# Optimization experiments

Hardware: AMD Instinct MI355X
Metric: run time of the kernel (lower is better)

## Reference

```python
import jax, jax.numpy as jnp
import numpy as np

IN_DIM = 135909   # input feature vocab (Amazon-670K style)
OUT_DIM = 670091  # output classes
D = 128           # hardcoded embedding dim in the module
B = 256           # batch size
T = 100           # active features per sample (summed bag-of-features)


def setup_inputs() -> dict:
    key = jax.random.key(0)
    ks = jax.random.split(key, 6)
    x = jax.random.randint(ks[0], (B, T), 0, IN_DIM)
    y = jax.random.randint(ks[1], (B,), 0, OUT_DIM)
    # nn.Embedding(IN+1, 128, padding_idx=IN): last row is the zero padding row
    emb_table = jax.random.normal(ks[2], (IN_DIM + 1, D), jnp.float32) * 0.01
    emb_table = emb_table.at[IN_DIM].set(0.0)
    stdv = 1.0 / np.sqrt(IN_DIM)
    bias = jax.random.uniform(ks[3], (D,), jnp.float32, -stdv, stdv)
    # LSHSoftmax dense parameters: per-class weight [OUT, D] and bias [OUT]
    W = jax.random.normal(ks[4], (OUT_DIM, D), jnp.float32) * (1.0 / np.sqrt(D))
    b_out = jnp.zeros((OUT_DIM,), jnp.float32)
    return {"x": x, "y": y, "freeze": 0, "slide": 0,
            "emb_table": emb_table, "bias": bias, "W": W, "b_out": b_out}


def reference(x, y, freeze, slide, emb_table, bias, W, b_out):
    # raw_emb = sum over the feature indices (bag-of-features embedding sum)
    raw = jnp.sum(emb_table[x], axis=1)                      # [B, D]
    emb = raw / jnp.linalg.norm(raw, axis=1, keepdims=True)  # L2 normalize
    query = jax.nn.relu(emb + bias)                          # [B, D]
    # LSHSoftmax exact (slide=0 / full) path: dense softmax cross-entropy
    logits = query @ W.T + b_out                             # [B, OUT]
    logp = jax.nn.log_softmax(logits, axis=-1)
    loss = -jnp.mean(jnp.take_along_axis(logp, y[:, None], axis=1))
    return loss
```

## Files before the change

kernel.cpp:

```cpp
#include <hip/hip_runtime.h>
#include <hip/hip_bf16.h>

#define IN_DIMX 135909
#define OUT_DIMX 670091
#define DDIM 128
#define BATCH 256
#define TFEAT 100
#define NBLK 512
#define NCHUNK ((OUT_DIMX + 63) / 64)

typedef __bf16 bf16_t;
typedef __attribute__((ext_vector_type(8))) __bf16 bf16x8;
typedef __attribute__((ext_vector_type(4))) __bf16 bf16x4;
typedef __attribute__((ext_vector_type(4))) float f32x4;

__global__ void k_query(const int* __restrict__ x, const float* __restrict__ emb,
                        const float* __restrict__ bias, float* __restrict__ qf,
                        bf16_t* __restrict__ qb) {
    const int row = blockIdx.x;
    const int t = threadIdx.x;
    __shared__ int sidx[TFEAT];
    if (t < TFEAT) sidx[t] = x[row * TFEAT + t];
    __syncthreads();
    float s = 0.f;
    #pragma unroll 10
    for (int i = 0; i < TFEAT; ++i) {
        s += emb[(size_t)sidx[i] * DDIM + t];
    }
    float sq = s * s;
    #pragma unroll
    for (int off = 1; off < 64; off <<= 1) sq += __shfl_xor(sq, off, 64);
    __shared__ float wred[2];
    if ((threadIdx.x & 63) == 0) wred[threadIdx.x >> 6] = sq;
    __syncthreads();
    const float tot = wred[0] + wred[1];
    float q = s / sqrtf(tot) + bias[t];
    q = fmaxf(q, 0.f);
    qf[row * DDIM + t] = q;
    qb[row * DDIM + t] = (bf16_t)q;
}

__global__ __launch_bounds__(256, 2)
void k_lse(const float* __restrict__ W, const float* __restrict__ b_out,
           const bf16_t* __restrict__ qb, float* __restrict__ partials) {
    __shared__ bf16_t lds[2][64 * DDIM];
    const int tid = threadIdx.x;
    const int lane = tid & 63;
    const int w = tid >> 6;
    const int l15 = lane & 15;
    const int l4 = lane >> 4;

    bf16x8 a[4][4];
    #pragma unroll
    for (int mt = 0; mt < 4; ++mt)
        #pragma unroll
        for (int ks = 0; ks < 4; ++ks)
            a[mt][ks] = *(const bf16x8*)(qb + (w * 64 + mt * 16 + l15) * DDIM + ks * 32 + 8 * l4);

    float rs[4][4];
    #pragma unroll
    for (int mt = 0; mt < 4; ++mt)
        #pragma unroll
        for (int r = 0; r < 4; ++r) rs[mt][r] = 0.f;

    const int srow = tid >> 5;
    const int scol = (tid & 31) * 4;
    const int c16  = (tid & 31) >> 1;
    const int half = (tid & 1) * 4;

    f32x4 wr[8];
    float bo_n[4];

    auto issue = [&](int ch) {
        const int cb = ch * 64;
        #pragma unroll
        for (int j = 0; j < 8; ++j) {
            int r = cb + j * 8 + srow;
            r = (r < OUT_DIMX) ? r : 0;
            wr[j] = *(const f32x4*)(W + (size_t)r * DDIM + scol);
        }
        #pragma unroll
        for (int nt = 0; nt < 4; ++nt) {
            int c = cb + nt * 16 + l15;
            c = (c < OUT_DIMX) ? c : 0;
            bo_n[nt] = b_out[c];
        }
    };

    auto convwrite = [&](int cur) {
        #pragma unroll
        for (int j = 0; j < 8; ++j) {
            const int row = j * 8 + srow;
            const int sp = row * 16 + (c16 ^ (row & 7));
            bf16x4 v;
            v[0] = (bf16_t)wr[j][0]; v[1] = (bf16_t)wr[j][1];
            v[2] = (bf16_t)wr[j][2]; v[3] = (bf16_t)wr[j][3];
            *(bf16x4*)(&lds[cur][sp * 8 + half]) = v;
        }
    };

    int cur = 0;
    issue(blockIdx.x);
    for (int ch = blockIdx.x; ch < NCHUNK; ch += NBLK) {
        float bo_c[4];
        #pragma unroll
        for (int nt = 0; nt < 4; ++nt) bo_c[nt] = bo_n[nt];

        convwrite(cur);
        __syncthreads();
        __builtin_amdgcn_sched_barrier(0);
        if (ch + NBLK < NCHUNK) issue(ch + NBLK);

        f32x4 acc[4][4];
        #pragma unroll
        for (int mt = 0; mt < 4; ++mt)
            #pragma unroll
            for (int nt = 0; nt < 4; ++nt) acc[mt][nt] = (f32x4){0.f, 0.f, 0.f, 0.f};

        #pragma unroll
        for (int ks = 0; ks < 4; ++ks) {
            bf16x8 b[4];
            #pragma unroll
            for (int nt = 0; nt < 4; ++nt) {
                const int row = nt * 16 + l15;
                const int sp = row * 16 + ((ks * 4 + l4) ^ (row & 7));
                b[nt] = *(const bf16x8*)(&lds[cur][sp * 8]);
            }
            #pragma unroll
            for (int nt = 0; nt < 4; ++nt)
                #pragma unroll
                for (int mt = 0; mt < 4; ++mt)
                    acc[mt][nt] = __builtin_amdgcn_mfma_f32_16x16x32_bf16(
                        a[mt][ks], b[nt], acc[mt][nt], 0, 0, 0);
        }

        const int cbase = ch * 64;
        if (cbase + 64 <= OUT_DIMX) {
            #pragma unroll
            for (int nt = 0; nt < 4; ++nt)
                #pragma unroll
                for (int mt = 0; mt < 4; ++mt)
                    #pragma unroll
                    for (int r = 0; r < 4; ++r)
                        rs[mt][r] += __expf(acc[mt][nt][r] + bo_c[nt]);
        } else {
            #pragma unroll
            for (int nt = 0; nt < 4; ++nt) {
                const bool valid = (cbase + nt * 16 + l15 < OUT_DIMX);
                #pragma unroll
                for (int mt = 0; mt < 4; ++mt)
                    #pragma unroll
                    for (int r = 0; r < 4; ++r)
                        rs[mt][r] += valid ? __expf(acc[mt][nt][r] + bo_c[nt]) : 0.f;
            }
        }
        cur ^= 1;
    }

    #pragma unroll
    for (int mt = 0; mt < 4; ++mt)
        #pragma unroll
        for (int r = 0; r < 4; ++r) {
            float v = rs[mt][r];
            v += __shfl_xor(v, 1, 64);
            v += __shfl_xor(v, 2, 64);
            v += __shfl_xor(v, 4, 64);
            v += __shfl_xor(v, 8, 64);
            if (l15 == 0) {
                const int rowb = w * 64 + mt * 16 + l4 * 4 + r;
                partials[(size_t)rowb * NBLK + blockIdx.x] = v;
            }
        }
}

__global__ void k_ydot(const int* __restrict__ y, const float* __restrict__ qf,
                       const float* __restrict__ W, const float* __restrict__ b_out,
                       float* __restrict__ logity) {
    const int i = blockIdx.x;
    const int lane = threadIdx.x;
    const int yi = y[i];
    const float* wrow = W + (size_t)yi * DDIM;
    const float* qrow = qf + i * DDIM;
    float s = qrow[lane] * wrow[lane] + qrow[lane + 64] * wrow[lane + 64];
    #pragma unroll
    for (int off = 1; off < 64; off <<= 1) s += __shfl_xor(s, off, 64);
    if (lane == 0) logity[i] = s + b_out[yi];
}

__global__ void k_rowlse(const float* __restrict__ partials,
                         const float* __restrict__ logity,
                         float* __restrict__ rowloss) {
    const int i = blockIdx.x;
    const int lane = threadIdx.x;
    float s = 0.f;
    #pragma unroll
    for (int k = 0; k < NBLK / 64; ++k)
        s += partials[(size_t)i * NBLK + k * 64 + lane];
    #pragma unroll
    for (int off = 1; off < 64; off <<= 1) s += __shfl_xor(s, off, 64);
    if (lane == 0) rowloss[i] = logf(s) - logity[i];
}

__global__ void k_final(const float* __restrict__ rowloss, float* __restrict__ out) {
    const int i = threadIdx.x;
    float t = rowloss[i];
    #pragma unroll
    for (int off = 1; off < 64; off <<= 1) t += __shfl_xor(t, off, 64);
    __shared__ float wred[4];
    if ((threadIdx.x & 63) == 0) wred[threadIdx.x >> 6] = t;
    __syncthreads();
    if (threadIdx.x == 0)
        out[0] = (wred[0] + wred[1] + wred[2] + wred[3]) * (1.0f / (float)BATCH);
}

extern "C" void kernel_launch(void* const* d_in, const int* in_sizes, int n_in,
                              void* d_out, int out_size, void* d_ws, size_t ws_size,
                              hipStream_t stream) {
    const int*   x     = (const int*)d_in[0];
    const int*   y     = (const int*)d_in[1];
    const float* emb   = (const float*)d_in[4];
    const float* bias  = (const float*)d_in[5];
    const float* W     = (const float*)d_in[6];
    const float* b_out = (const float*)d_in[7];
    float* out = (float*)d_out;

    char* ws = (char*)d_ws;
    bf16_t* qb       = (bf16_t*)(ws);
    float*  qf       = (float*)(ws + 65536);
    float*  logity   = (float*)(ws + 196608);
    float*  rowloss  = (float*)(ws + 197632);
    float*  partials = (float*)(ws + 262144);

    k_query<<<BATCH, DDIM, 0, stream>>>(x, emb, bias, qf, qb);
    k_ydot<<<BATCH, 64, 0, stream>>>(y, qf, W, b_out, logity);
    k_lse<<<NBLK, 256, 0, stream>>>(W, b_out, qb, partials);
    k_rowlse<<<BATCH, 64, 0, stream>>>(partials, logity, rowloss);
    k_final<<<1, 256, 0, stream>>>(rowloss, out);
}
```

Baseline: 90.65 us.

## Deepen W prefetch to two register sets and fuse ydot into rowlse

```diff
diff --git a/kernel.cpp b/kernel.cpp
--- a/kernel.cpp
+++ b/kernel.cpp
@@ -68,10 +68,10 @@
     const int c16  = (tid & 31) >> 1;
     const int half = (tid & 1) * 4;
 
-    f32x4 wr[8];
-    float bo_n[4];
-
-    auto issue = [&](int ch) {
+    f32x4 wrA[8], wrB[8];
+    float boA[4], boB[4];
+
+    auto issue = [&](int ch, f32x4 (&wr)[8], float (&bo)[4]) {
         const int cb = ch * 64;
         #pragma unroll
         for (int j = 0; j < 8; ++j) {
@@ -81,13 +81,13 @@
         }
         #pragma unroll
         for (int nt = 0; nt < 4; ++nt) {
-            int c = cb + nt * 16 + l15;
-            c = (c < OUT_DIMX) ? c : 0;
-            bo_n[nt] = b_out[c];
+            int cc = cb + nt * 16 + l15;
+            cc = (cc < OUT_DIMX) ? cc : 0;
+            bo[nt] = b_out[cc];
         }
     };
 
-    auto convwrite = [&](int cur) {
+    auto convwrite = [&](int buf, f32x4 (&wr)[8]) {
         #pragma unroll
         for (int j = 0; j < 8; ++j) {
             const int row = j * 8 + srow;
@@ -95,22 +95,11 @@
             bf16x4 v;
             v[0] = (bf16_t)wr[j][0]; v[1] = (bf16_t)wr[j][1];
             v[2] = (bf16_t)wr[j][2]; v[3] = (bf16_t)wr[j][3];
-            *(bf16x4*)(&lds[cur][sp * 8 + half]) = v;
+            *(bf16x4*)(&lds[buf][sp * 8 + half]) = v;
         }
     };
 
-    int cur = 0;
-    issue(blockIdx.x);
-    for (int ch = blockIdx.x; ch < NCHUNK; ch += NBLK) {
-        float bo_c[4];
-        #pragma unroll
-        for (int nt = 0; nt < 4; ++nt) bo_c[nt] = bo_n[nt];
-
-        convwrite(cur);
-        __syncthreads();
-        __builtin_amdgcn_sched_barrier(0);
-        if (ch + NBLK < NCHUNK) issue(ch + NBLK);
-
+    auto compute = [&](int buf, int ch, const float (&boc)[4]) {
         f32x4 acc[4][4];
         #pragma unroll
         for (int mt = 0; mt < 4; ++mt)
@@ -119,19 +108,16 @@
 
         #pragma unroll
         for (int ks = 0; ks < 4; ++ks) {
-            bf16x8 b[4];
             #pragma unroll
             for (int nt = 0; nt < 4; ++nt) {
                 const int row = nt * 16 + l15;
                 const int sp = row * 16 + ((ks * 4 + l4) ^ (row & 7));
-                b[nt] = *(const bf16x8*)(&lds[cur][sp * 8]);
-            }
-            #pragma unroll
-            for (int nt = 0; nt < 4; ++nt)
+                const bf16x8 b = *(const bf16x8*)(&lds[buf][sp * 8]);
                 #pragma unroll
                 for (int mt = 0; mt < 4; ++mt)
                     acc[mt][nt] = __builtin_amdgcn_mfma_f32_16x16x32_bf16(
-                        a[mt][ks], b[nt], acc[mt][nt], 0, 0, 0);
+                        a[mt][ks], b, acc[mt][nt], 0, 0, 0);
+            }
         }
 
         const int cbase = ch * 64;
@@ -142,7 +128,7 @@
                 for (int mt = 0; mt < 4; ++mt)
                     #pragma unroll
                     for (int r = 0; r < 4; ++r)
-                        rs[mt][r] += __expf(acc[mt][nt][r] + bo_c[nt]);
+                        rs[mt][r] += __expf(acc[mt][nt][r] + boc[nt]);
         } else {
             #pragma unroll
             for (int nt = 0; nt < 4; ++nt) {
@@ -151,10 +137,41 @@
                 for (int mt = 0; mt < 4; ++mt)
                     #pragma unroll
                     for (int r = 0; r < 4; ++r)
-                        rs[mt][r] += valid ? __expf(acc[mt][nt][r] + bo_c[nt]) : 0.f;
+                        rs[mt][r] += valid ? __expf(acc[mt][nt][r] + boc[nt]) : 0.f;
             }
         }
-        cur ^= 1;
+    };
+
+    int c = blockIdx.x;
+    issue(c, wrA, boA);
+    {
+        const int c1 = c + NBLK;
+        issue(c1 < NCHUNK ? c1 : c, wrB, boB);
+    }
+    for (; c < NCHUNK; c += 2 * NBLK) {
+        {
+            const float boc[4] = {boA[0], boA[1], boA[2], boA[3]};
+            convwrite(0, wrA);
+            asm volatile("s_waitcnt lgkmcnt(0)" ::: "memory");
+            __builtin_amdgcn_sched_barrier(0);
+            __builtin_amdgcn_s_barrier();
+            __builtin_amdgcn_sched_barrier(0);
+            const int cn = c + 2 * NBLK;
+            issue(cn < NCHUNK ? cn : 0, wrA, boA);
+            compute(0, c, boc);
+        }
+        const int cB = c + NBLK;
+        if (cB < NCHUNK) {
+            const float boc[4] = {boB[0], boB[1], boB[2], boB[3]};
+            convwrite(1, wrB);
+            asm volatile("s_waitcnt lgkmcnt(0)" ::: "memory");
+            __builtin_amdgcn_sched_barrier(0);
+            __builtin_amdgcn_s_barrier();
+            __builtin_amdgcn_sched_barrier(0);
+            const int cn = cB + 2 * NBLK;
+            issue(cn < NCHUNK ? cn : 0, wrB, boB);
+            compute(1, cB, boc);
+        }
     }
 
     #pragma unroll
@@ -173,22 +190,11 @@
         }
 }
 
-__global__ void k_ydot(const int* __restrict__ y, const float* __restrict__ qf,
-                       const float* __restrict__ W, const float* __restrict__ b_out,
-                       float* __restrict__ logity) {
-    const int i = blockIdx.x;
-    const int lane = threadIdx.x;
-    const int yi = y[i];
-    const float* wrow = W + (size_t)yi * DDIM;
-    const float* qrow = qf + i * DDIM;
-    float s = qrow[lane] * wrow[lane] + qrow[lane + 64] * wrow[lane + 64];
-    #pragma unroll
-    for (int off = 1; off < 64; off <<= 1) s += __shfl_xor(s, off, 64);
-    if (lane == 0) logity[i] = s + b_out[yi];
-}
-
 __global__ void k_rowlse(const float* __restrict__ partials,
-                         const float* __restrict__ logity,
+                         const int* __restrict__ y,
+                         const float* __restrict__ qf,
+                         const float* __restrict__ W,
+                         const float* __restrict__ b_out,
                          float* __restrict__ rowloss) {
     const int i = blockIdx.x;
     const int lane = threadIdx.x;
@@ -196,9 +202,16 @@
     #pragma unroll
     for (int k = 0; k < NBLK / 64; ++k)
         s += partials[(size_t)i * NBLK + k * 64 + lane];
-    #pragma unroll
-    for (int off = 1; off < 64; off <<= 1) s += __shfl_xor(s, off, 64);
-    if (lane == 0) rowloss[i] = logf(s) - logity[i];
+    const int yi = y[i];
+    const float* wrow = W + (size_t)yi * DDIM;
+    const float* qrow = qf + i * DDIM;
+    float d = qrow[lane] * wrow[lane] + qrow[lane + 64] * wrow[lane + 64];
+    #pragma unroll
+    for (int off = 1; off < 64; off <<= 1) {
+        s += __shfl_xor(s, off, 64);
+        d += __shfl_xor(d, off, 64);
+    }
+    if (lane == 0) rowloss[i] = logf(s) - (d + b_out[yi]);
 }
 
 __global__ void k_final(const float* __restrict__ rowloss, float* __restrict__ out) {
@@ -227,13 +240,11 @@
     char* ws = (char*)d_ws;
     bf16_t* qb       = (bf16_t*)(ws);
     float*  qf       = (float*)(ws + 65536);
-    float*  logity   = (float*)(ws + 196608);
     float*  rowloss  = (float*)(ws + 197632);
     float*  partials = (float*)(ws + 262144);
 
     k_query<<<BATCH, DDIM, 0, stream>>>(x, emb, bias, qf, qb);
-    k_ydot<<<BATCH, 64, 0, stream>>>(y, qf, W, b_out, logity);
     k_lse<<<NBLK, 256, 0, stream>>>(W, b_out, qb, partials);
-    k_rowlse<<<BATCH, 64, 0, stream>>>(partials, logity, rowloss);
+    k_rowlse<<<BATCH, 64, 0, stream>>>(partials, y, qf, W, b_out, rowloss);
     k_final<<<1, 256, 0, stream>>>(rowloss, out);
 }
```

After: 117.5 us. 1.3x slower.
